# Kernel tuning notes

Measured on AMD Instinct MI355X. Metric: run time of the kernel, lower is better.

The kernel has to match this reference:

```python
import jax, jax.numpy as jnp
import numpy as np
import itertools

# ---- static config (mirrors args in init_kwargs) ----
BS = 4                        # num_processes
H, W = 480, 640               # frame_height, frame_width
NC = 16                       # num_sem_categories
C = 4 + NC                    # obs channels: RGB + depth + semantics
RES = 5                       # map_resolution (cm per cell)
ZRES = 5
MAP_CM = 4800 // 2            # map_size_cm // global_downscaling
M = MAP_CM // RES             # 480 local-map cells
VR = 100                      # vision_range
FOV = 79.0                    # hfov (deg)
DU = 1                        # du_scale
AGENT_H = 1.55 * 100.0        # camera_height * 100 (cm)
MAXH = int(360 / ZRES)        # 72
MINH = int(-40 / ZRES)        # -8
ZH = MAXH - MINH              # 80 height bins
MAP_THR, EXP_THR, CAT_THR = 1.0, 1.0, 5.0
DEG = 57.29577951308232
MIN_Z = int(5 / ZRES - MINH)                    # 9
MAX_Z = int((AGENT_H + 1 + 50) / ZRES - MINH)   # 49
XCAM = (W - 1.0) / 2.0
ZCAM = (H - 1.0) / 2.0
FOC = (W / 2.0) / np.tan(np.deg2rad(FOV / 2.0))


def _splat_feat_nd(feat, coords, grid_dims):
    # feat: (B,F,N) ; coords: (B,3,N) normalized to [-1,1] ; trilinear scatter-add
    B, Fc, N = feat.shape
    G = grid_dims[0] * grid_dims[1] * grid_dims[2]
    grid_flat = jnp.zeros((B, Fc, G), feat.dtype)
    pos_dim, wts_dim = [], []
    for d in range(3):
        gd = grid_dims[d]
        pos = coords[:, d, :] * (gd / 2.0) + gd / 2.0   # (B,N) voxel-space coord
        fl = jnp.floor(pos)
        pd, wd = [], []
        for ix in (0.0, 1.0):
            pos_ix = fl + ix
            safe = ((pos_ix > 0) & (pos_ix < gd)).astype(feat.dtype)
            wd.append((1.0 - jnp.abs(pos - pos_ix)) * safe)
            pd.append(pos_ix * safe)  # unsafe points dumped at index 0 with weight 0
        pos_dim.append(pd)
        wts_dim.append(wd)
    for ix_d in itertools.product((0, 1), (0, 1), (0, 1)):
        w = wts_dim[0][ix_d[0]] * wts_dim[1][ix_d[1]] * wts_dim[2][ix_d[2]]
        idx = jnp.zeros_like(w)
        for d in range(3):
            idx = idx * grid_dims[d] + pos_dim[d][ix_d[d]]
        idx = idx.astype(jnp.int32)                     # (B,N)
        vals = feat * w[:, None, :]                     # (B,F,N)
        grid_flat = jax.vmap(lambda g, i, v: g.at[:, i].add(v))(grid_flat, idx, vals)
    grid_flat = jnp.round(grid_flat)
    return grid_flat.reshape((B, Fc) + tuple(grid_dims))


def _affine_grid(theta, Hh, Ww):
    # align_corners=True base grid
    xs = jnp.linspace(-1.0, 1.0, Ww)
    ys = jnp.linspace(-1.0, 1.0, Hh)
    Xg, Yg = jnp.meshgrid(xs, ys)
    base = jnp.stack([Xg, Yg, jnp.ones_like(Xg)], -1)   # (H,W,3)
    return jnp.einsum('bij,hwj->bhwi', theta, base)     # (B,H,W,2)


def _grid_sample(img, grid):
    # bilinear, align_corners=True, zero padding; img (B,C,H,W), grid (B,Ho,Wo,2)
    B, Cc, Hh, Ww = img.shape
    x = (grid[..., 0] + 1.0) * 0.5 * (Ww - 1)
    y = (grid[..., 1] + 1.0) * 0.5 * (Hh - 1)
    x0 = jnp.floor(x)
    y0 = jnp.floor(y)
    wx1 = x - x0
    wy1 = y - y0

    def gather(ix, iy):
        valid = ((ix >= 0) & (ix <= Ww - 1) & (iy >= 0) & (iy <= Hh - 1)).astype(img.dtype)
        ixc = jnp.clip(ix, 0, Ww - 1).astype(jnp.int32)
        iyc = jnp.clip(iy, 0, Hh - 1).astype(jnp.int32)
        v = jax.vmap(lambda im, yy, xx: im[:, yy, xx])(img, iyc, ixc)  # (B,C,Ho,Wo)
        return v * valid[:, None]

    return (gather(x0, y0) * ((1 - wx1) * (1 - wy1))[:, None]
            + gather(x0 + 1, y0) * (wx1 * (1 - wy1))[:, None]
            + gather(x0, y0 + 1) * ((1 - wx1) * wy1)[:, None]
            + gather(x0 + 1, y0 + 1) * (wx1 * wy1)[:, None])


def _forward(obs, pose_obs, maps_last, poses_last, view_angles):
    bs = obs.shape[0]
    depth = obs[:, 3, ::DU, ::DU]                        # (B,h,w) depth in cm
    gx = jnp.arange(W, dtype=obs.dtype)[None, None, ::DU]
    gz = jnp.arange(H - 1, -1, -1, dtype=obs.dtype)[None, ::DU, None]
    Xp = (gx - XCAM) * depth / FOC
    Zp = (gz - ZCAM) * depth / FOC
    # rotate about x-axis by per-env view angle (deg), then lift by agent height
    a = jnp.deg2rad(view_angles)[:, None, None]
    ca, sa = jnp.cos(a), jnp.sin(a)
    Xv = Xp
    Yv = ca * depth - sa * Zp
    Zv = sa * depth + ca * Zp + AGENT_H
    # shift_loc rotation angle is pi/2 - pi/2 = 0 -> identity rot, only x shift
    Xv = Xv + VR * RES / 2.0
    # normalize to [-1,1] voxel coords
    xs = (Xv / RES - VR // 2.0) / VR * 2.0
    ys = (Yv / RES - VR // 2.0) / VR * 2.0
    zs = (Zv / ZRES - (MAXH + MINH) // 2.0) / (MAXH - MINH) * 2.0
    coords = jnp.stack([xs, ys, zs], 1).reshape(bs, 3, -1)   # (B,3,N)
    # features: channel 0 = ones (occupancy), rest = avg-pooled semantic masks
    sem = obs[:, 4:]
    pooled = sem.reshape(bs, NC, H // DU, DU, W // DU, DU).mean((3, 5))
    N = (H // DU) * (W // DU)
    feat = jnp.concatenate([jnp.ones((bs, 1, N), obs.dtype), pooled.reshape(bs, NC, N)], 1)
    voxels = _splat_feat_nd(feat, coords, (VR, VR, ZH)).swapaxes(2, 3)  # (B,1+NC,VR,VR,ZH)
    agg = voxels[..., MIN_Z:MAX_Z].sum(4)
    fp_map_pred = jnp.clip(agg[:, :1] / MAP_THR, 0.0, 1.0)
    fp_exp_pred = jnp.clip(voxels.sum(4)[:, :1] / EXP_THR, 0.0, 1.0)
    cat_pred = jnp.clip(agg[:, 1:] / CAT_THR, 0.0, 1.0)
    agent_view = jnp.zeros((bs, C, M, M), obs.dtype)
    x1 = M // 2 - VR // 2
    x2 = x1 + VR
    y1 = M // 2
    y2 = y1 + VR
    agent_view = agent_view.at[:, 0:1, y1:y2, x1:x2].set(fp_map_pred)
    agent_view = agent_view.at[:, 1:2, y1:y2, x1:x2].set(fp_exp_pred)
    agent_view = agent_view.at[:, 4:, y1:y2, x1:x2].set(cat_pred)
    # pose integration (get_new_pose_batch, note sequential in-place semantics)
    o = poses_last[:, 2] / DEG
    yy = poses_last[:, 1] + pose_obs[:, 0] * jnp.sin(o) + pose_obs[:, 1] * jnp.cos(o)
    xx = poses_last[:, 0] + pose_obs[:, 0] * jnp.cos(o) - pose_obs[:, 1] * jnp.sin(o)
    tt = poses_last[:, 2] + pose_obs[:, 2] * DEG
    tt = jnp.fmod(tt - 180.0, 360.0) + 180.0
    tt = jnp.fmod(tt + 180.0, 360.0) - 180.0
    current_poses = jnp.stack([xx, yy, tt], 1)
    # st_pose is detached in the original
    st = jax.lax.stop_gradient(current_poses)
    half = M // 2
    stx = -(st[:, 0] * 100.0 / RES - half) / half
    sty = -(st[:, 1] * 100.0 / RES - half) / half
    t = (90.0 - st[:, 2]) * np.pi / 180.0
    ct, s_t = jnp.cos(t), jnp.sin(t)
    zero, one = jnp.zeros_like(ct), jnp.ones_like(ct)
    theta1 = jnp.stack([jnp.stack([ct, -s_t, zero], 1), jnp.stack([s_t, ct, zero], 1)], 1)
    theta2 = jnp.stack([jnp.stack([one, zero, stx], 1), jnp.stack([zero, one, sty], 1)], 1)
    rotated = _grid_sample(agent_view, _affine_grid(theta1, M, M))
    translated = _grid_sample(rotated, _affine_grid(theta2, M, M))
    map_pred = jnp.maximum(maps_last, translated)
    # pose_pred aliases the in-place-updated poses_last in torch == current_poses
    return fp_map_pred, map_pred, current_poses, current_poses, translated


def setup_inputs() -> dict:
    key = jax.random.key(0)
    k1, k2, k3, k4 = jax.random.split(key, 4)
    obs = jax.random.uniform(k1, (BS, C, H, W), jnp.float32)
    obs = obs.at[:, 3].multiply(400.0)  # depth channel in cm, up to 4 m
    pose_obs = jax.random.uniform(k2, (BS, 3), jnp.float32) * 0.25
    maps_last = jax.random.uniform(k3, (BS, C, M, M), jnp.float32)
    poses_last = jax.random.uniform(k4, (BS, 3), jnp.float32)
    view_angles = jnp.zeros((BS,), jnp.float32)
    return {"obs": obs, "pose_obs": pose_obs, "maps_last": maps_last,
            "poses_last": poses_last, "view_angles": view_angles}


def reference(obs, pose_obs, maps_last, poses_last, view_angles):
    return _forward(obs, pose_obs, maps_last, poses_last, view_angles)
```

## Files before the change

### kernel.cpp

```cpp
#include <hip/hip_runtime.h>
#include <math.h>

#define BS 4
#define HH 480
#define WW 640
#define NPX (HH * WW)
#define NC 16
#define CHN 20
#define MM 480
#define VRD 100
#define ZHD 80
#define MINZ 9
#define MAXZ 49
#define CAP 8192

#define OFF0 0
#define OFF1 40000
#define OFF2 18472000
#define OFF3 18472012
#define OFF4 18472024
#define OFFM 28840000
#define OFFC 36113600
#define OFFS 36120000
#define RECOFF 40000

__device__ __forceinline__ void pix2pos(int w, int h, float depth, float ca, float sa,
                                        float foc, float& px, float& py, float& pz) {
    float gx = (float)w;
    float gz = (float)(HH - 1 - h);
    float Xp = (gx - 319.5f) * depth / foc;
    float Zp = (gz - 239.5f) * depth / foc;
    float Yv = ca * depth - sa * Zp;
    float Zv = sa * depth + ca * Zp + 155.0f;
    float Xv = Xp + 250.0f;
    float xs = (Xv / 5.0f - 50.0f) / 100.0f * 2.0f;
    float ys = (Yv / 5.0f - 50.0f) / 100.0f * 2.0f;
    float zs = (Zv / 5.0f - 32.0f) / 80.0f * 2.0f;
    px = xs * 50.0f + 50.0f;
    py = ys * 50.0f + 50.0f;
    pz = zs * 40.0f + 40.0f;
}

__global__ __launch_bounds__(256) void bin_kernel(const float* __restrict__ obs,
                                                  const float* __restrict__ va,
                                                  int* __restrict__ cnt,
                                                  float2* __restrict__ rec,
                                                  float foc) {
    int idx = blockIdx.x * blockDim.x + threadIdx.x;
    if (idx >= BS * NPX) return;
    int b   = idx / NPX;
    int rem = idx % NPX;
    float depth = obs[((size_t)b * CHN + 3) * NPX + rem];
    int h = rem / WW, w = rem % WW;
    float a  = va[b] * 0.017453292519943295f;
    float ca = cosf(a), sa = sinf(a);
    float px, py, pz;
    pix2pos(w, h, depth, ca, sa, foc, px, py, pz);
    int f = (int)floorf(py);
    if (f < 0 || f > 99) return;
    int slot = atomicAdd(cnt + (b * VRD + f) * 16, 1);
    if (slot < CAP) {
        float2 r; r.x = __int_as_float(rem); r.y = depth;
        rec[(size_t)(b * VRD + f) * CAP + slot] = r;
    }
}

__global__ __launch_bounds__(256, 6) void slice_kernel(const float* __restrict__ obs,
                                                       const int* __restrict__ cnt,
                                                       const float2* __restrict__ rec,
                                                       const float* __restrict__ va,
                                                       float* __restrict__ maps,
                                                       float* __restrict__ stage,
                                                       float foc) {
    __shared__ float acc[40 * VRD];
    int bid  = blockIdx.x;
    int wgid = (bid & 7) * 900 + (bid >> 3);
    int b  = wgid / 1800;
    int r_ = wgid % 1800;
    int c  = r_ / 100;
    int s  = r_ % 100;
    int tid = threadIdx.x;
    for (int i = tid; i < 40 * VRD; i += 256) acc[i] = 0.0f;
    __syncthreads();

    bool isocc = (c >= 16);
    float clo   = isocc ? ((c == 16) ? 1.0f : 40.0f) : 9.0f;
    float chi   = isocc ? ((c == 16) ? 40.0f : 80.0f) : 49.0f;
    int   zbase = isocc ? ((c == 16) ? 0 : 40) : 9;
    const float* sb = isocc ? (const float*)0 : obs + ((size_t)b * CHN + 4 + c) * NPX;

    float a  = va[b] * 0.017453292519943295f;
    float ca = cosf(a), sa = sinf(a);
    int sm1 = (s > 0) ? s - 1 : 0;
    int n0 = (s > 0) ? min(cnt[(b * VRD + sm1) * 16], CAP) : 0;
    int n1 = min(cnt[(b * VRD + s) * 16], CAP);
    const float2* g0 = rec + (size_t)(b * VRD + sm1) * CAP;
    const float2* g1 = rec + (size_t)(b * VRD + s) * CAP;
    int N = (s == 0) ? 0 : n0 + n1;
    float fs = (float)s;

    int nblk = (N + 1023) >> 10;
    for (int blk = 0; blk < nblk; blk++) {
        int base = (blk << 10) + tid;
        float2 rv[4]; bool vld[4];
        #pragma unroll
        for (int j = 0; j < 4; j++) {
            int t = base + (j << 8);
            vld[j] = (t < N);
            rv[j] = vld[j] ? ((t < n0) ? g0[t] : g1[t - n0]) : make_float2(0.0f, 0.0f);
        }
        int rm[4]; float px[4], py[4], pz[4]; bool act[4];
        #pragma unroll
        for (int j = 0; j < 4; j++) {
            rm[j] = __float_as_int(rv[j].x);
            pix2pos(rm[j] % WW, rm[j] / WW, rv[j].y, ca, sa, foc, px[j], py[j], pz[j]);
            float wy = 1.0f - fabsf(py[j] - fs);
            bool ok = vld[j] && (wy > 0.0f);
            ok = ok && (pz[j] > clo - 1.0f) && (pz[j] < chi);
            float fx = floorf(px[j]);
            ok = ok && (fx + 1.0f > 0.0f) && (fx < 100.0f);
            act[j] = ok;
        }
        float sv[4];
        #pragma unroll
        for (int j = 0; j < 4; j++)
            sv[j] = (!isocc && act[j]) ? sb[rm[j]] : 1.0f;
        #pragma unroll
        for (int j = 0; j < 4; j++) {
            if (!act[j]) continue;
            float wy = 1.0f - fabsf(py[j] - fs);
            float fx = floorf(px[j]), fz = floorf(pz[j]);
            #pragma unroll
            for (int i2 = 0; i2 < 2; i2++) {
                float cxp = fx + (float)i2;
                if (!(cxp > 0.0f && cxp < 100.0f)) continue;
                float wxy = wy * (1.0f - fabsf(px[j] - cxp));
                int xi = (int)cxp;
                #pragma unroll
                for (int k = 0; k < 2; k++) {
                    float czp = fz + (float)k;
                    if (czp < clo || czp >= chi) continue;
                    float w3 = wxy * (1.0f - fabsf(pz[j] - czp));
                    if (w3 == 0.0f) continue;
                    atomicAdd(&acc[((int)czp - zbase) * VRD + xi], w3 * sv[j]);
                }
            }
        }
    }
    __syncthreads();

    if (!isocc) {
        for (int x = tid; x < VRD; x += 256) {
            float ssum = 0.0f;
            #pragma unroll 8
            for (int z = 0; z < 40; z++) ssum += rintf(acc[z * VRD + x]);
            maps[((size_t)(b * 18 + 2 + c) * VRD + s) * VRD + x] =
                fminf(fmaxf(ssum * 0.2f, 0.0f), 1.0f);
        }
    } else {
        int cell0 = (c == 16) ? 0 : 40;
        for (int x = tid; x < VRD; x += 256) {
            float s_all = 0.0f, s_agg = 0.0f;
            #pragma unroll 8
            for (int z = 0; z < 40; z++) {
                float r = rintf(acc[z * VRD + x]);
                s_all += r;
                int cell = cell0 + z;
                if (cell >= MINZ && cell < MAXZ) s_agg += r;
            }
            int o = (b * VRD + s) * VRD + x;
            atomicAdd(stage + o, s_all);
            atomicAdd(stage + 40000 + o, s_agg);
        }
    }
}

__global__ __launch_bounds__(256) void fixup_kernel(const float* __restrict__ stage,
                                                    float* __restrict__ maps,
                                                    float* __restrict__ out0) {
    int idx = blockIdx.x * blockDim.x + threadIdx.x;
    if (idx >= BS * VRD * VRD) return;
    int b = idx / (VRD * VRD);
    int r = idx % (VRD * VRD);
    float all = stage[idx];
    float agg = stage[40000 + idx];
    float fm = fminf(fmaxf(agg, 0.0f), 1.0f);
    float fe = fminf(fmaxf(all, 0.0f), 1.0f);
    maps[(size_t)(b * 18 + 0) * 10000 + r] = fm;
    maps[(size_t)(b * 18 + 1) * 10000 + r] = fe;
    out0[idx] = fm;
}

__device__ __forceinline__ void pose_params(const float* __restrict__ pose_obs,
                                            const float* __restrict__ poses_last,
                                            int b, float& ct, float& st,
                                            float& stx, float& sty) {
    const float DEG = 57.29577951308232f;
    float o  = poses_last[b*3+2] / DEG;
    float so = sinf(o), co = cosf(o);
    float yy = poses_last[b*3+1] + pose_obs[b*3+0]*so + pose_obs[b*3+1]*co;
    float xx = poses_last[b*3+0] + pose_obs[b*3+0]*co - pose_obs[b*3+1]*so;
    float tt = poses_last[b*3+2] + pose_obs[b*3+2]*DEG;
    tt = fmodf(tt - 180.0f, 360.0f) + 180.0f;
    tt = fmodf(tt + 180.0f, 360.0f) - 180.0f;
    stx = -((xx*100.0f/5.0f) - 240.0f) / 240.0f;
    sty = -((yy*100.0f/5.0f) - 240.0f) / 240.0f;
    float t = (90.0f - tt) * 0.017453292519943295f;
    ct = cosf(t); st = sinf(t);
}

__global__ __launch_bounds__(64) void pose_kernel(const float* __restrict__ pose_obs,
                                                  const float* __restrict__ poses_last,
                                                  float* __restrict__ out) {
    int b = threadIdx.x;
    if (b >= BS) return;
    const float DEG = 57.29577951308232f;
    float o  = poses_last[b*3+2] / DEG;
    float so = sinf(o), co = cosf(o);
    float yy = poses_last[b*3+1] + pose_obs[b*3+0]*so + pose_obs[b*3+1]*co;
    float xx = poses_last[b*3+0] + pose_obs[b*3+0]*co - pose_obs[b*3+1]*so;
    float tt = poses_last[b*3+2] + pose_obs[b*3+2]*DEG;
    tt = fmodf(tt - 180.0f, 360.0f) + 180.0f;
    tt = fmodf(tt + 180.0f, 360.0f) - 180.0f;
    out[OFF2 + b*3+0] = xx; out[OFF2 + b*3+1] = yy; out[OFF2 + b*3+2] = tt;
    out[OFF3 + b*3+0] = xx; out[OFF3 + b*3+1] = yy; out[OFF3 + b*3+2] = tt;
}

__global__ __launch_bounds__(256) void rotate_kernel(const float* __restrict__ maps,
                                                     const float* __restrict__ pose_obs,
                                                     const float* __restrict__ poses_last,
                                                     float* __restrict__ rot) {
    int idx = blockIdx.x * blockDim.x + threadIdx.x;
    if (idx >= BS * MM * MM) return;
    int b   = idx / (MM * MM);
    int rem = idx % (MM * MM);
    int y   = rem / MM;
    int x   = rem % MM;
    float ct, st, stx, sty;
    pose_params(pose_obs, poses_last, b, ct, st, stx, sty);
    float Xg = -1.0f + (float)x * (2.0f / 479.0f);
    float Yg = -1.0f + (float)y * (2.0f / 479.0f);
    float gx = ct * Xg - st * Yg;
    float gy = st * Xg + ct * Yg;
    float xf = (gx + 1.0f) * 0.5f * 479.0f;
    float yf = (gy + 1.0f) * 0.5f * 479.0f;
    float x0 = floorf(xf), y0 = floorf(yf);
    float fx = xf - x0, fy = yf - y0;
    float cw[4] = {(1.0f - fx) * (1.0f - fy), fx * (1.0f - fy),
                   (1.0f - fx) * fy,          fx * fy};
    float cx[4] = {x0, x0 + 1.0f, x0, x0 + 1.0f};
    float cy[4] = {y0, y0, y0 + 1.0f, y0 + 1.0f};
    float acc[18];
    #pragma unroll
    for (int m = 0; m < 18; m++) acc[m] = 0.0f;
    #pragma unroll
    for (int k = 0; k < 4; k++) {
        float fxk = cx[k], fyk = cy[k];
        if (!(fxk >= 0.0f && fxk <= 479.0f && fyk >= 0.0f && fyk <= 479.0f)) continue;
        int ix = (int)fxk, iy = (int)fyk;
        if (iy < 240 || iy >= 340 || ix < 190 || ix >= 290) continue;
        int mi = iy - 240, mj = ix - 190;
        float w = cw[k];
        const float* mp = maps + (size_t)b * 18 * VRD * VRD + mi * VRD + mj;
        #pragma unroll
        for (int m = 0; m < 18; m++) acc[m] += w * mp[(size_t)m * VRD * VRD];
    }
    size_t obase = ((size_t)b * CHN) * MM * MM + (size_t)y * MM + x;
    rot[obase + (size_t)0 * MM * MM] = acc[0];
    rot[obase + (size_t)1 * MM * MM] = acc[1];
    rot[obase + (size_t)2 * MM * MM] = 0.0f;
    rot[obase + (size_t)3 * MM * MM] = 0.0f;
    #pragma unroll
    for (int m = 2; m < 18; m++)
        rot[obase + (size_t)(m + 2) * MM * MM] = acc[m];
}

__global__ __launch_bounds__(256) void translate_kernel(const float* __restrict__ rot,
                                                        const float* __restrict__ pose_obs,
                                                        const float* __restrict__ poses_last,
                                                        float* __restrict__ tr) {
    int idx = blockIdx.x * blockDim.x + threadIdx.x;
    if (idx >= BS * MM * MM) return;
    int b   = idx / (MM * MM);
    int rem = idx % (MM * MM);
    int y   = rem / MM;
    int x   = rem % MM;
    float ct, st, stx, sty;
    pose_params(pose_obs, poses_last, b, ct, st, stx, sty);
    float Xg = -1.0f + (float)x * (2.0f / 479.0f);
    float Yg = -1.0f + (float)y * (2.0f / 479.0f);
    float xf = (Xg + stx + 1.0f) * 0.5f * 479.0f;
    float yf = (Yg + sty + 1.0f) * 0.5f * 479.0f;
    float x0 = floorf(xf), y0 = floorf(yf);
    float fx = xf - x0, fy = yf - y0;
    float cw[4] = {(1.0f - fx) * (1.0f - fy), fx * (1.0f - fy),
                   (1.0f - fx) * fy,          fx * fy};
    float cxs[4] = {x0, x0 + 1.0f, x0, x0 + 1.0f};
    float cys[4] = {y0, y0, y0 + 1.0f, y0 + 1.0f};
    bool vk[4]; int offk[4];
    #pragma unroll
    for (int k = 0; k < 4; k++) {
        vk[k] = (cxs[k] >= 0.0f && cxs[k] <= 479.0f && cys[k] >= 0.0f && cys[k] <= 479.0f);
        offk[k] = vk[k] ? ((int)cys[k] * MM + (int)cxs[k]) : 0;
    }
    #pragma unroll
    for (int c = 0; c < CHN; c++) {
        const float* rp = rot + ((size_t)b * CHN + c) * MM * MM;
        float v = 0.0f;
        #pragma unroll
        for (int k = 0; k < 4; k++)
            if (vk[k]) v += cw[k] * rp[offk[k]];
        tr[((size_t)b * CHN + c) * MM * MM + (size_t)y * MM + x] = v;
    }
}

__global__ __launch_bounds__(256) void max_kernel(const float* __restrict__ maps_last,
                                                  const float* __restrict__ tr,
                                                  float* __restrict__ mp) {
    int i = blockIdx.x * blockDim.x + threadIdx.x;
    int n4 = BS * CHN * MM * MM / 4;
    if (i >= n4) return;
    float4 a = ((const float4*)maps_last)[i];
    float4 t = ((const float4*)tr)[i];
    float4 r;
    r.x = fmaxf(a.x, t.x);
    r.y = fmaxf(a.y, t.y);
    r.z = fmaxf(a.z, t.z);
    r.w = fmaxf(a.w, t.w);
    ((float4*)mp)[i] = r;
}

extern "C" void kernel_launch(void* const* d_in, const int* in_sizes, int n_in,
                              void* d_out, int out_size, void* d_ws, size_t ws_size,
                              hipStream_t stream) {
    const float* obs         = (const float*)d_in[0];
    const float* pose_obs    = (const float*)d_in[1];
    const float* maps_last   = (const float*)d_in[2];
    const float* poses_last  = (const float*)d_in[3];
    const float* view_angles = (const float*)d_in[4];
    float* out = (float*)d_out;

    float*  maps  = out + OFFM;
    float2* rec   = (float2*)(out + RECOFF);
    int*    cnt   = (int*)(out + OFFC);
    float*  stage = out + OFFS;

    hipMemsetAsync(cnt, 0, (6400 + 80000) * sizeof(float), stream);

    const float foc = (float)(320.0 / tan(39.5 * M_PI / 180.0));

    int npix = BS * NPX;
    bin_kernel<<<(npix + 255) / 256, 256, 0, stream>>>(obs, view_angles, cnt, rec, foc);

    slice_kernel<<<dim3(VRD * BS * 18), 256, 0, stream>>>(obs, cnt, rec, view_angles,
                                                          maps, stage, foc);

    fixup_kernel<<<(BS * VRD * VRD + 255) / 256, 256, 0, stream>>>(stage, maps, out + OFF0);

    pose_kernel<<<1, 64, 0, stream>>>(pose_obs, poses_last, out);

    int nmap = BS * MM * MM;
    rotate_kernel<<<(nmap + 255) / 256, 256, 0, stream>>>(maps, pose_obs, poses_last,
                                                          out + OFF1);
    translate_kernel<<<(nmap + 255) / 256, 256, 0, stream>>>(out + OFF1, pose_obs,
                                                             poses_last, out + OFF4);
    int n4 = BS * CHN * MM * MM / 4;
    max_kernel<<<(n4 + 255) / 256, 256, 0, stream>>>(maps_last, out + OFF4, out + OFF1);
}
```

Before: 1.243 ms.

## Process two semantic channels per slice block and fuse occupancy fixup

Each slice workgroup now accumulates two semantic channels together in an interleaved shared-memory buffer, and the two occupancy height halves are merged into one 80-bin block. This halves the number of workgroups, so each block's records and projections are recomputed half as often. Because each occupancy block now covers the full height range, the staging buffer, its atomics, its memset and the separate fixup kernel are removed. In exchange, shared memory per block doubles (8000 floats), occupancy drops from 6 to 5 blocks per CU, and the occupancy blocks do more serial work.

New measurement: 1.299 ms. 4.6% more time.

```diff
diff --git a/kernel.cpp b/kernel.cpp
--- a/kernel.cpp
+++ b/kernel.cpp
@@ -21,7 +21,6 @@
 #define OFF4 18472024
 #define OFFM 28840000
 #define OFFC 36113600
-#define OFFS 36120000
 #define RECOFF 40000
 
 __device__ __forceinline__ void pix2pos(int w, int h, float depth, float ca, float sa,
@@ -65,29 +64,29 @@
     }
 }
 
-__global__ __launch_bounds__(256, 6) void slice_kernel(const float* __restrict__ obs,
+__global__ __launch_bounds__(256, 5) void slice_kernel(const float* __restrict__ obs,
                                                        const int* __restrict__ cnt,
                                                        const float2* __restrict__ rec,
                                                        const float* __restrict__ va,
                                                        float* __restrict__ maps,
-                                                       float* __restrict__ stage,
+                                                       float* __restrict__ out0,
                                                        float foc) {
-    __shared__ float acc[40 * VRD];
+    __shared__ float acc[8000];
     int bid  = blockIdx.x;
-    int wgid = (bid & 7) * 900 + (bid >> 3);
-    int b  = wgid / 1800;
-    int r_ = wgid % 1800;
-    int c  = r_ / 100;
+    int wgid = (bid & 7) * 450 + (bid >> 3);
+    int b  = wgid / 900;
+    int r_ = wgid % 900;
+    int g  = r_ / 100;
     int s  = r_ % 100;
     int tid = threadIdx.x;
-    for (int i = tid; i < 40 * VRD; i += 256) acc[i] = 0.0f;
+    for (int i = tid; i < 8000; i += 256) acc[i] = 0.0f;
     __syncthreads();
 
-    bool isocc = (c >= 16);
-    float clo   = isocc ? ((c == 16) ? 1.0f : 40.0f) : 9.0f;
-    float chi   = isocc ? ((c == 16) ? 40.0f : 80.0f) : 49.0f;
-    int   zbase = isocc ? ((c == 16) ? 0 : 40) : 9;
-    const float* sb = isocc ? (const float*)0 : obs + ((size_t)b * CHN + 4 + c) * NPX;
+    bool isocc = (g == 8);
+    float clo = isocc ? 1.0f : 9.0f;
+    float chi = isocc ? 80.0f : 49.0f;
+    int zbase = isocc ? 0 : 9;
+    const float* sb = isocc ? (const float*)0 : obs + ((size_t)b * CHN + 4 + 2 * g) * NPX;
 
     float a  = va[b] * 0.017453292519943295f;
     float ca = cosf(a), sa = sinf(a);
@@ -121,10 +120,13 @@
             ok = ok && (fx + 1.0f > 0.0f) && (fx < 100.0f);
             act[j] = ok;
         }
-        float sv[4];
-        #pragma unroll
-        for (int j = 0; j < 4; j++)
-            sv[j] = (!isocc && act[j]) ? sb[rm[j]] : 1.0f;
+        float sv0[4], sv1[4];
+        #pragma unroll
+        for (int j = 0; j < 4; j++) {
+            bool gth = !isocc && act[j];
+            sv0[j] = gth ? sb[rm[j]] : 1.0f;
+            sv1[j] = gth ? sb[rm[j] + NPX] : 1.0f;
+        }
         #pragma unroll
         for (int j = 0; j < 4; j++) {
             if (!act[j]) continue;
@@ -142,7 +144,14 @@
                     if (czp < clo || czp >= chi) continue;
                     float w3 = wxy * (1.0f - fabsf(pz[j] - czp));
                     if (w3 == 0.0f) continue;
-                    atomicAdd(&acc[((int)czp - zbase) * VRD + xi], w3 * sv[j]);
+                    int zi = (int)czp - zbase;
+                    if (isocc) {
+                        atomicAdd(&acc[zi * VRD + xi], w3);
+                    } else {
+                        float* dst = &acc[(zi * VRD + xi) * 2];
+                        atomicAdd(dst + 0, w3 * sv0[j]);
+                        atomicAdd(dst + 1, w3 * sv1[j]);
+                    }
                 }
             }
         }
@@ -150,45 +159,30 @@
     __syncthreads();
 
     if (!isocc) {
-        for (int x = tid; x < VRD; x += 256) {
+        for (int i = tid; i < VRD * 2; i += 256) {
+            int x = i >> 1, c = i & 1;
             float ssum = 0.0f;
             #pragma unroll 8
-            for (int z = 0; z < 40; z++) ssum += rintf(acc[z * VRD + x]);
-            maps[((size_t)(b * 18 + 2 + c) * VRD + s) * VRD + x] =
+            for (int z = 0; z < 40; z++) ssum += rintf(acc[(z * VRD + x) * 2 + c]);
+            maps[((size_t)(b * 18 + 2 + 2 * g + c) * VRD + s) * VRD + x] =
                 fminf(fmaxf(ssum * 0.2f, 0.0f), 1.0f);
         }
     } else {
-        int cell0 = (c == 16) ? 0 : 40;
         for (int x = tid; x < VRD; x += 256) {
             float s_all = 0.0f, s_agg = 0.0f;
             #pragma unroll 8
-            for (int z = 0; z < 40; z++) {
+            for (int z = 0; z < ZHD; z++) {
                 float r = rintf(acc[z * VRD + x]);
                 s_all += r;
-                int cell = cell0 + z;
-                if (cell >= MINZ && cell < MAXZ) s_agg += r;
+                if (z >= MINZ && z < MAXZ) s_agg += r;
             }
-            int o = (b * VRD + s) * VRD + x;
-            atomicAdd(stage + o, s_all);
-            atomicAdd(stage + 40000 + o, s_agg);
-        }
-    }
-}
-
-__global__ __launch_bounds__(256) void fixup_kernel(const float* __restrict__ stage,
-                                                    float* __restrict__ maps,
-                                                    float* __restrict__ out0) {
-    int idx = blockIdx.x * blockDim.x + threadIdx.x;
-    if (idx >= BS * VRD * VRD) return;
-    int b = idx / (VRD * VRD);
-    int r = idx % (VRD * VRD);
-    float all = stage[idx];
-    float agg = stage[40000 + idx];
-    float fm = fminf(fmaxf(agg, 0.0f), 1.0f);
-    float fe = fminf(fmaxf(all, 0.0f), 1.0f);
-    maps[(size_t)(b * 18 + 0) * 10000 + r] = fm;
-    maps[(size_t)(b * 18 + 1) * 10000 + r] = fe;
-    out0[idx] = fm;
+            float fm = fminf(fmaxf(s_agg, 0.0f), 1.0f);
+            float fe = fminf(fmaxf(s_all, 0.0f), 1.0f);
+            maps[((size_t)(b * 18 + 0) * VRD + s) * VRD + x] = fm;
+            maps[((size_t)(b * 18 + 1) * VRD + s) * VRD + x] = fe;
+            out0[((size_t)b * VRD + s) * VRD + x] = fm;
+        }
+    }
 }
 
 __device__ __forceinline__ void pose_params(const float* __restrict__ pose_obs,
@@ -343,19 +337,16 @@
     float*  maps  = out + OFFM;
     float2* rec   = (float2*)(out + RECOFF);
     int*    cnt   = (int*)(out + OFFC);
-    float*  stage = out + OFFS;
-
-    hipMemsetAsync(cnt, 0, (6400 + 80000) * sizeof(float), stream);
+
+    hipMemsetAsync(cnt, 0, 6400 * sizeof(int), stream);
 
     const float foc = (float)(320.0 / tan(39.5 * M_PI / 180.0));
 
     int npix = BS * NPX;
     bin_kernel<<<(npix + 255) / 256, 256, 0, stream>>>(obs, view_angles, cnt, rec, foc);
 
-    slice_kernel<<<dim3(VRD * BS * 18), 256, 0, stream>>>(obs, cnt, rec, view_angles,
-                                                          maps, stage, foc);
-
-    fixup_kernel<<<(BS * VRD * VRD + 255) / 256, 256, 0, stream>>>(stage, maps, out + OFF0);
+    slice_kernel<<<dim3(VRD * BS * 9), 256, 0, stream>>>(obs, cnt, rec, view_angles,
+                                                         maps, out + OFF0, foc);
 
     pose_kernel<<<1, 64, 0, stream>>>(pose_obs, poses_last, out);
 
```
